# Kernel tuning notes

Hardware: AMD Instinct MI355X
Metric: run time of the kernel (lower is better)

## Reference

```python
import jax, jax.numpy as jnp
import numpy as np

D_MODEL = 1024
N_LAYER = 2
VOCAB = 50257
D_STATE = 64
D_CONV = 4
EXPAND = 2
HEADDIM = 64
D_INNER = EXPAND * D_MODEL            # 2048
NHEADS = D_INNER // HEADDIM           # 32
CONV_DIM = D_INNER + 2 * D_STATE      # x, B, C share the conv (ngroups=1)
D_PROJ = 2 * D_INNER + 2 * D_STATE + NHEADS  # z, xBC, dt
D_FF = 4 * D_MODEL
B, T = 1, 1024
EPS = 1e-5


def _layernorm(x, w):
    mu = jnp.mean(x, -1, keepdims=True)
    v = jnp.mean((x - mu) ** 2, -1, keepdims=True)
    return (x - mu) * jax.lax.rsqrt(v + EPS) * w


def _rmsnorm(x, w):
    return x * jax.lax.rsqrt(jnp.mean(x ** 2, -1, keepdims=True) + EPS) * w


def setup_inputs() -> dict:
    key = jax.random.key(0)
    ks = jax.random.split(key, 16)
    std = 0.02
    idx = jax.random.randint(ks[0], (B, T), 0, VOCAB)
    targets = jax.random.randint(ks[1], (B, T), 0, VOCAB)
    E = jax.random.normal(ks[2], (VOCAB, D_MODEL)) * std  # tied embedding / lm_head
    norm_w = jnp.ones((N_LAYER, D_MODEL))
    norm2_w = jnp.ones((N_LAYER, D_MODEL))
    norm_f_w = jnp.ones((D_MODEL,))
    in_proj_w = jax.random.normal(ks[3], (N_LAYER, D_PROJ, D_MODEL)) * std
    conv_w = jax.random.normal(ks[4], (N_LAYER, CONV_DIM, D_CONV)) / np.sqrt(D_CONV)
    conv_b = jnp.zeros((N_LAYER, CONV_DIM))
    dt = jnp.exp(jax.random.uniform(ks[5], (N_LAYER, NHEADS)) * (np.log(0.1) - np.log(1e-3)) + np.log(1e-3))
    dt_bias = dt + jnp.log(-jnp.expm1(-dt))  # inverse softplus
    A_log = jnp.log(jax.random.uniform(ks[6], (N_LAYER, NHEADS), minval=1.0, maxval=16.0))
    Dp = jnp.ones((N_LAYER, NHEADS))
    gnorm_w = jnp.ones((N_LAYER, D_INNER))
    out_proj_w = jax.random.normal(ks[7], (N_LAYER, D_MODEL, D_INNER)) * std / np.sqrt(2 * N_LAYER)
    fc1_w = jax.random.normal(ks[8], (N_LAYER, 2 * D_FF, D_MODEL)) * std
    fc2_w = jax.random.normal(ks[9], (N_LAYER, D_MODEL, D_FF)) * std / np.sqrt(2 * N_LAYER)
    return {"idx": idx, "targets": targets, "E": E, "norm_w": norm_w, "norm2_w": norm2_w,
            "in_proj_w": in_proj_w, "conv_w": conv_w, "conv_b": conv_b, "dt_bias": dt_bias,
            "A_log": A_log, "Dp": Dp, "gnorm_w": gnorm_w, "out_proj_w": out_proj_w,
            "fc1_w": fc1_w, "fc2_w": fc2_w, "norm_f_w": norm_f_w}


def _mamba2(x, Wi, cw, cb, dtb, Al, Dh, gw, Wo):
    b, l, _ = x.shape
    zxbcdt = x @ Wi.T  # [b,l,D_PROJ]
    z = zxbcdt[..., :D_INNER]
    xBC = zxbcdt[..., D_INNER:D_INNER + CONV_DIM]
    dt = zxbcdt[..., D_INNER + CONV_DIM:]  # [b,l,H]
    # depthwise causal conv1d over time
    xp = jnp.pad(xBC, ((0, 0), (D_CONV - 1, 0), (0, 0)))
    xBC = sum(xp[:, k:k + l, :] * cw[:, k] for k in range(D_CONV)) + cb
    xBC = jax.nn.silu(xBC)
    xs = xBC[..., :D_INNER].reshape(b, l, NHEADS, HEADDIM)
    Bm = xBC[..., D_INNER:D_INNER + D_STATE]  # [b,l,N] (ngroups=1)
    Cm = xBC[..., D_INNER + D_STATE:]
    dt = jax.nn.softplus(dt + dtb)            # [b,l,H]
    dA = jnp.exp(dt * (-jnp.exp(Al)))         # [b,l,H]
    tm = lambda a: jnp.moveaxis(a, 1, 0)      # time-major for scan

    def step(h, inp):
        dA_t, dt_t, x_t, B_t, C_t = inp
        h = dA_t[..., None, None] * h + jnp.einsum('bh,bhp,bn->bhpn', dt_t, x_t, B_t)
        return h, jnp.einsum('bhpn,bn->bhp', h, C_t)

    h0 = jnp.zeros((b, NHEADS, HEADDIM, D_STATE), x.dtype)
    _, ys = jax.lax.scan(step, h0, (tm(dA), tm(dt), tm(xs), tm(Bm), tm(Cm)))
    y = jnp.moveaxis(ys, 0, 1) + Dh[None, None, :, None] * xs  # skip term D*x
    y = y.reshape(b, l, D_INNER)
    y = _rmsnorm(y * jax.nn.silu(z), gw)  # gated RMSNorm
    return y @ Wo.T


def _gated_mlp(x, W1, W2):
    y = x @ W1.T
    y, g = jnp.split(y, 2, axis=-1)
    return (y * jax.nn.silu(g)) @ W2.T


def reference(idx, targets, E, norm_w, norm2_w, in_proj_w, conv_w, conv_b, dt_bias,
              A_log, Dp, gnorm_w, out_proj_w, fc1_w, fc2_w, norm_f_w):
    h = E[idx]  # [B,T,D]
    for i in range(N_LAYER):
        x = _layernorm(h, norm_w[i])
        x = _mamba2(x, in_proj_w[i], conv_w[i], conv_b[i], dt_bias[i], A_log[i],
                    Dp[i], gnorm_w[i], out_proj_w[i])
        res = x + h
        x = _layernorm(res, norm2_w[i])
        h = _gated_mlp(x, fc1_w[i], fc2_w[i]) + res
    h = _layernorm(h, norm_f_w)
    logits = h @ E.T  # tied lm_head
    logp = jax.nn.log_softmax(logits, axis=-1)
    nll = -jnp.take_along_axis(logp, targets[..., None], axis=-1)[..., 0]
    loss = jnp.mean(nll)  # no ignore_index=-1 entries present
    return logits, loss
```

## Files before the change

kernel.cpp:

```cpp
#include <hip/hip_runtime.h>
#include <cmath>

#define DMODEL  1024
#define DINNER  2048
#define NHEADS  32
#define CONVDIM 2176
#define DPROJ   4256
#define VOCAB   50257
#define NBLK_V  400
#define VOCABP  (NBLK_V * 128)
#define CLEN    16
#define NCHUNK  64

typedef float f32x4 __attribute__((ext_vector_type(4)));
typedef float f32x2 __attribute__((ext_vector_type(2)));
typedef unsigned short u16;
typedef u16 u16x4 __attribute__((ext_vector_type(4)));
typedef u16 u16x8 __attribute__((ext_vector_type(8)));
typedef __bf16 bf16x8 __attribute__((ext_vector_type(8)));

__device__ __forceinline__ u16 f2bf(float f) {
  unsigned u = __builtin_bit_cast(unsigned, f);
  u += 0x7FFFu + ((u >> 16) & 1u);
  return (u16)(u >> 16);
}
__device__ __forceinline__ float silu_f(float x) { return x / (1.f + expf(-x)); }

__device__ __forceinline__ void gload16(const u16* g, u16* l) {
  __builtin_amdgcn_global_load_lds(
      (const __attribute__((address_space(1))) void*)g,
      (__attribute__((address_space(3))) void*)l,
      16, 0, 0);
}

__global__ __launch_bounds__(256) void gemm_bf16(
    const u16* __restrict__ A, const u16* __restrict__ B,
    float* __restrict__ C, int N, int K, int kslice,
    float* __restrict__ lsepart, int swz, int nblk,
    u16* __restrict__ glu_out)
{
  __shared__ alignas(128) u16 As[2][128 * 64];
  __shared__ alignas(128) u16 Bs[2][128 * 64];
  const int tid = threadIdx.x;
  int m0, n0;
  if (swz) {
    int bid = blockIdx.x;
    m0 = ((bid >> 3) & 7) << 7;
    n0 = ((bid & 7) + ((bid >> 6) << 3)) << 7;
  } else {
    m0 = blockIdx.x << 7;
    n0 = blockIdx.y << 7;
  }
  const int lane = tid & 63, wid = tid >> 6;
  const int wm = (wid >> 1) << 6, wn = (wid & 1) << 6;
  const int lr = lane & 15, kg = lane >> 4;

  const int srow = wid * 8 + (lane >> 3);
  const int scol = ((lane & 7) ^ (lane >> 3)) << 3;
  const u16* gA = A + (size_t)(m0 + srow) * K + scol;
  const u16* gB = B + (size_t)(n0 + srow) * K + scol;

  f32x4 acc[4][4];
#pragma unroll
  for (int i = 0; i < 4; ++i)
#pragma unroll
    for (int j = 0; j < 4; ++j) acc[i][j] = (f32x4){0.f, 0.f, 0.f, 0.f};

  const int kb = blockIdx.z * kslice;
  const int nt = kslice >> 6;

  auto stage = [&](int buf, int kk) {
#pragma unroll
    for (int i = 0; i < 4; ++i) {
      gload16(gA + kk + (size_t)i * 32 * K, &As[buf][i * 2048 + wid * 512]);
      gload16(gB + kk + (size_t)i * 32 * K, &Bs[buf][i * 2048 + wid * 512]);
    }
  };

  stage(0, kb);
  asm volatile("s_waitcnt vmcnt(0)" ::: "memory");
  __builtin_amdgcn_s_barrier();

  int cur = 0;
  for (int t = 0; t < nt; ++t) {
    if (t + 1 < nt) stage(cur ^ 1, kb + (t + 1) * 64);
#pragma unroll
    for (int kk = 0; kk < 2; ++kk) {
      bf16x8 af[4], bfr[4];
      const int cx = ((kk * 4 + kg) ^ (lr & 7)) << 3;
#pragma unroll
      for (int f = 0; f < 4; ++f) {
        af[f]  = *(const bf16x8*)&As[cur][(wm + f * 16 + lr) * 64 + cx];
        bfr[f] = *(const bf16x8*)&Bs[cur][(wn + f * 16 + lr) * 64 + cx];
      }
#pragma unroll
      for (int i = 0; i < 4; ++i)
#pragma unroll
        for (int j = 0; j < 4; ++j)
          acc[i][j] = __builtin_amdgcn_mfma_f32_16x16x32_bf16(af[i], bfr[j], acc[i][j], 0, 0, 0);
    }
    asm volatile("s_waitcnt vmcnt(0)" ::: "memory");
    __builtin_amdgcn_s_barrier();
    cur ^= 1;
  }

  const int mr = (lane >> 4) << 2;
  const int nc = lane & 15;

  if (glu_out) {
#pragma unroll
    for (int i = 0; i < 4; ++i)
#pragma unroll
      for (int j = 0; j < 4; ++j)
#pragma unroll
        for (int e = 0; e < 4; ++e) {
          float v = acc[i][j][e];
          float p = __shfl_xor(v, 1);
          if (!(nc & 1)) {
            int q = (n0 + wn + j * 16 + nc) >> 1;
            int row = m0 + wm + i * 16 + mr + e;
            glu_out[(size_t)row * 4096 + q] = f2bf(v * silu_f(p));
          }
        }
    return;
  }

  float* Cw = C + (gridDim.z > 1 ? (size_t)blockIdx.z * 1024 * N : 0);
#pragma unroll
  for (int i = 0; i < 4; ++i)
#pragma unroll
    for (int j = 0; j < 4; ++j) {
      int n = n0 + wn + j * 16 + nc;
      if (n < N) {
#pragma unroll
        for (int e = 0; e < 4; ++e)
          Cw[(size_t)(m0 + wm + i * 16 + mr + e) * N + n] = acc[i][j][e];
      }
    }

  if (lsepart) {
    float* Ls = (float*)As;
#pragma unroll
    for (int i = 0; i < 4; ++i)
#pragma unroll
      for (int e = 0; e < 4; ++e) {
        float pm = -1e30f;
#pragma unroll
        for (int j = 0; j < 4; ++j) {
          int n = n0 + wn + j * 16 + nc;
          if (n < N) pm = fmaxf(pm, acc[i][j][e]);
        }
#pragma unroll
        for (int o = 1; o < 16; o <<= 1) pm = fmaxf(pm, __shfl_xor(pm, o));
        float ps = 0.f;
#pragma unroll
        for (int j = 0; j < 4; ++j) {
          int n = n0 + wn + j * 16 + nc;
          if (n < N) ps += expf(acc[i][j][e] - pm);
        }
#pragma unroll
        for (int o = 1; o < 16; o <<= 1) ps += __shfl_xor(ps, o);
        if (nc == 0) {
          int row = wm + i * 16 + mr + e;
          Ls[row * 4 + (wid & 1) * 2] = pm;
          Ls[row * 4 + (wid & 1) * 2 + 1] = ps;
        }
      }
    __syncthreads();
    if (tid < 128) {
      float pa = Ls[tid * 4], sa = Ls[tid * 4 + 1];
      float pb = Ls[tid * 4 + 2], sb = Ls[tid * 4 + 3];
      float M = fmaxf(pa, pb);
      float S = sa * expf(pa - M) + sb * expf(pb - M);
      ((f32x2*)lsepart)[(size_t)(m0 + tid) * nblk + (n0 >> 7)] = (f32x2){M, S};
    }
  }
}

__global__ void k_cvt8(const float* __restrict__ src, u16* __restrict__ dst, int n8) {
  int i = blockIdx.x * 256 + threadIdx.x;
  if (i >= n8) return;
  f32x4 a = ((const f32x4*)src)[i * 2];
  f32x4 b = ((const f32x4*)src)[i * 2 + 1];
  u16x8 o = { f2bf(a[0]), f2bf(a[1]), f2bf(a[2]), f2bf(a[3]),
              f2bf(b[0]), f2bf(b[1]), f2bf(b[2]), f2bf(b[3]) };
  ((u16x8*)dst)[i] = o;
}

__global__ void k_cvt8_pad(const float* __restrict__ src, u16* __restrict__ dst,
                           int n8, int srcN8) {
  int i = blockIdx.x * 256 + threadIdx.x;
  if (i >= n8) return;
  u16x8 o;
  if (i < srcN8) {
    f32x4 a = ((const f32x4*)src)[i * 2];
    f32x4 b = ((const f32x4*)src)[i * 2 + 1];
    o = (u16x8){ f2bf(a[0]), f2bf(a[1]), f2bf(a[2]), f2bf(a[3]),
                 f2bf(b[0]), f2bf(b[1]), f2bf(b[2]), f2bf(b[3]) };
  } else {
    o = (u16x8){0, 0, 0, 0, 0, 0, 0, 0};
  }
  ((u16x8*)dst)[i] = o;
}

__global__ void k_cvt_fc1(const float* __restrict__ src, u16* __restrict__ dst, int n8) {
  int i = blockIdx.x * 256 + threadIdx.x;
  if (i >= n8) return;
  f32x4 a = ((const f32x4*)src)[i * 2];
  f32x4 b = ((const f32x4*)src)[i * 2 + 1];
  u16x8 o = { f2bf(a[0]), f2bf(a[1]), f2bf(a[2]), f2bf(a[3]),
              f2bf(b[0]), f2bf(b[1]), f2bf(b[2]), f2bf(b[3]) };
  int R = i >> 7, col8 = i & 127;
  int layer = R >> 13, r = R & 8191;
  int dstr = (r < 4096) ? (r << 1) : (((r - 4096) << 1) | 1);
  ((u16x8*)dst)[((size_t)(layer << 13) + dstr) * 128 + col8] = o;
}

__device__ __forceinline__ void ln_write(f32x4 v, const float* __restrict__ w,
                                         u16* __restrict__ out, int t, int tid) {
  float s = v[0] + v[1] + v[2] + v[3];
  float sq = v[0]*v[0] + v[1]*v[1] + v[2]*v[2] + v[3]*v[3];
#pragma unroll
  for (int o = 32; o; o >>= 1) { s += __shfl_down(s, o); sq += __shfl_down(sq, o); }
  __shared__ float sb[4], qb[4];
  if ((tid & 63) == 0) { sb[tid >> 6] = s; qb[tid >> 6] = sq; }
  __syncthreads();
  s = sb[0] + sb[1] + sb[2] + sb[3];
  sq = qb[0] + qb[1] + qb[2] + qb[3];
  float mu = s * (1.f / 1024.f);
  float rstd = rsqrtf(sq * (1.f / 1024.f) - mu * mu + 1e-5f);
  u16x4 o;
#pragma unroll
  for (int e = 0; e < 4; ++e) o[e] = f2bf((v[e] - mu) * rstd * w[tid * 4 + e]);
  ((u16x4*)out)[t * 256 + tid] = o;
}

__global__ void k_ln_embed(const int* __restrict__ idx, const float* __restrict__ E,
                           const float* __restrict__ w, float* __restrict__ hbuf,
                           u16* __restrict__ out) {
  int t = blockIdx.x, tid = threadIdx.x;
  f32x4 v = ((const f32x4*)(E + (size_t)idx[t] * DMODEL))[tid];
  ((f32x4*)hbuf)[t * 256 + tid] = v;
  ln_write(v, w, out, t, tid);
}

__global__ void k_red_ln(const float* __restrict__ part, int S,
                         float* __restrict__ hbuf, const float* __restrict__ w,
                         u16* __restrict__ out) {
  int t = blockIdx.x, tid = threadIdx.x;
  f32x4 v = ((const f32x4*)hbuf)[t * 256 + tid];
  for (int k = 0; k < S; ++k)
    v += ((const f32x4*)part)[(size_t)k * 262144 + t * 256 + tid];
  ((f32x4*)hbuf)[t * 256 + tid] = v;
  ln_write(v, w, out, t, tid);
}

__global__ void k_convdt(const float* __restrict__ zx, const float* __restrict__ cw,
                         const float* __restrict__ cb, const float* __restrict__ dtb,
                         const float* __restrict__ alog, float* __restrict__ xbc,
                         float* __restrict__ dtsp, float* __restrict__ dag) {
  int t = blockIdx.y, x = blockIdx.x, tid = threadIdx.x;
  if (x < 8 || tid < 128) {
    int c = x * 256 + tid;
    float acc = cb[c];
#pragma unroll
    for (int k = 0; k < 4; ++k) {
      int tt = t + k - 3;
      if (tt >= 0) acc += zx[(size_t)tt * DPROJ + 2048 + c] * cw[c * 4 + k];
    }
    xbc[(size_t)t * CONVDIM + c] = silu_f(acc);
  } else if (tid < 160) {
    int hh = tid - 128;
    float raw = zx[(size_t)t * DPROJ + 4224 + hh] + dtb[hh];
    float sp = raw > 20.f ? raw : log1pf(expf(raw));
    dtsp[t * 32 + hh] = sp;
    dag[t * 32 + hh] = expf(-expf(alog[hh]) * sp);
  }
}

__global__ __launch_bounds__(256) void k_scan_local(
    const float* __restrict__ xbc, const float* __restrict__ dtsp,
    const float* __restrict__ dag, float* __restrict__ yb, float* __restrict__ Sloc,
    float* __restrict__ pref, float* __restrict__ dacum)
{
  int c = blockIdx.x, hh = blockIdx.y;
  int tid = threadIdx.x;
  int p = tid >> 2, ng = tid & 3, n0 = ng << 4;
  float st[16];
#pragma unroll
  for (int j = 0; j < 16; ++j) st[j] = 0.f;
  float P = 1.f;
  for (int s_ = 0; s_ < CLEN; ++s_) {
    int t = c * CLEN + s_;
    float dA = dag[t * 32 + hh];
    P *= dA;
    if (tid == 0) pref[t * 32 + hh] = P;
    float coef = dtsp[t * 32 + hh] * xbc[(size_t)t * CONVDIM + hh * 64 + p];
    const f32x4* B4 = (const f32x4*)&xbc[(size_t)t * CONVDIM + 2048 + n0];
    const f32x4* C4 = (const f32x4*)&xbc[(size_t)t * CONVDIM + 2112 + n0];
    float y = 0.f;
#pragma unroll
    for (int q = 0; q < 4; ++q) {
      f32x4 b = B4[q], cc = C4[q];
#pragma unroll
      for (int e = 0; e < 4; ++e) {
        int j = q * 4 + e;
        st[j] = dA * st[j] + coef * b[e];
        y += st[j] * cc[e];
      }
    }
    y += __shfl_xor(y, 1);
    y += __shfl_xor(y, 2);
    if (ng == 0) yb[(size_t)t * DINNER + hh * 64 + p] = y;
  }
  if (tid == 0) dacum[c * 32 + hh] = P;
  float* Sp = Sloc + ((size_t)(c * 32 + hh) * 64 + p) * 64 + n0;
#pragma unroll
  for (int q = 0; q < 4; ++q)
    *(f32x4*)(Sp + q * 4) = (f32x4){ st[q*4], st[q*4+1], st[q*4+2], st[q*4+3] };
}

__global__ void k_chain(const float* __restrict__ Sloc, const float* __restrict__ dacum,
                        float* __restrict__ Sin) {
  int e = blockIdx.x * 256 + threadIdx.x;
  int hh = e >> 12;
  float S = 0.f;
  for (int c = 0; c < NCHUNK; ++c) {
    Sin[(size_t)c * 131072 + e] = S;
    S = dacum[c * 32 + hh] * S + Sloc[(size_t)c * 131072 + e];
  }
}

__global__ __launch_bounds__(256) void k_scan_fix(
    const float* __restrict__ xbc, const float* __restrict__ pref,
    const float* __restrict__ Sin, const float* __restrict__ Dp,
    float* __restrict__ yb)
{
  __shared__ float Sl[64 * 68];
  int c = blockIdx.x, hh = blockIdx.y;
  int tid = threadIdx.x;
  for (int i = 0; i < 16; ++i) {
    int e = i * 256 + tid;
    Sl[(e >> 6) * 68 + (e & 63)] = Sin[(size_t)(c * 32 + hh) * 4096 + e];
  }
  __syncthreads();
  int p = tid >> 2, ng = tid & 3, n0 = ng << 4;
  float Dh = Dp[hh];
  for (int s_ = 0; s_ < CLEN; ++s_) {
    int t = c * CLEN + s_;
    const f32x4* C4 = (const f32x4*)&xbc[(size_t)t * CONVDIM + 2112 + n0];
    float yc = 0.f;
#pragma unroll
    for (int q = 0; q < 4; ++q) {
      f32x4 cc = C4[q];
#pragma unroll
      for (int e = 0; e < 4; ++e) yc += Sl[p * 68 + n0 + q * 4 + e] * cc[e];
    }
    yc += __shfl_xor(yc, 1);
    yc += __shfl_xor(yc, 2);
    if (ng == 0) {
      size_t oy = (size_t)t * DINNER + hh * 64 + p;
      yb[oy] = yb[oy] + pref[t * 32 + hh] * yc + Dh * xbc[(size_t)t * CONVDIM + hh * 64 + p];
    }
  }
}

__global__ void k_gated_rms(const float* __restrict__ yb, const float* __restrict__ zx,
                            const float* __restrict__ gw, u16* __restrict__ out) {
  int t = blockIdx.x, tid = threadIdx.x;
  float v[8], ss = 0.f;
#pragma unroll
  for (int i = 0; i < 8; ++i) {
    int j = tid + i * 256;
    float z = zx[(size_t)t * DPROJ + j];
    float vv = yb[(size_t)t * DINNER + j] * silu_f(z);
    v[i] = vv; ss += vv * vv;
  }
#pragma unroll
  for (int o = 32; o; o >>= 1) ss += __shfl_down(ss, o);
  __shared__ float sb[4];
  if ((tid & 63) == 0) sb[tid >> 6] = ss;
  __syncthreads();
  ss = sb[0] + sb[1] + sb[2] + sb[3];
  float rstd = rsqrtf(ss * (1.f / 2048.f) + 1e-5f);
#pragma unroll
  for (int i = 0; i < 8; ++i) {
    int j = tid + i * 256;
    out[(size_t)t * DINNER + j] = f2bf(v[i] * rstd * gw[j]);
  }
}

__global__ void k_loss_final(const float* __restrict__ lsepart,
                             const float* __restrict__ logits,
                             const int* __restrict__ tgt, float* __restrict__ part) {
  int t = blockIdx.x, tid = threadIdx.x;
  float m = -1e30f, s = 0.f;
  for (int nb = tid; nb < NBLK_V; nb += 256) {
    f32x2 v = ((const f32x2*)lsepart)[(size_t)t * NBLK_V + nb];
    float M = fmaxf(m, v[0]);
    s = s * expf(m - M) + v[1] * expf(v[0] - M);
    m = M;
  }
#pragma unroll
  for (int o = 32; o; o >>= 1) {
    float m2 = __shfl_down(m, o), s2 = __shfl_down(s, o);
    float M = fmaxf(m, m2);
    s = s * expf(m - M) + s2 * expf(m2 - M);
    m = M;
  }
  __shared__ float ms[4], ssh[4];
  if ((tid & 63) == 0) { ms[tid >> 6] = m; ssh[tid >> 6] = s; }
  __syncthreads();
  if (tid == 0) {
    float M = ms[0], S = ssh[0];
    for (int w = 1; w < 4; ++w) {
      float M2 = fmaxf(M, ms[w]);
      S = S * expf(M - M2) + ssh[w] * expf(ms[w] - M2);
      M = M2;
    }
    part[t] = (M + logf(S)) - logits[(size_t)t * VOCAB + tgt[t]];
  }
}

__global__ void k_loss_mean(const float* __restrict__ part, float* __restrict__ out) {
  int tid = threadIdx.x;
  float s = 0.f;
  for (int j = tid; j < 1024; j += 256) s += part[j];
#pragma unroll
  for (int o = 32; o; o >>= 1) s += __shfl_down(s, o);
  __shared__ float sb[4];
  if ((tid & 63) == 0) sb[tid >> 6] = s;
  __syncthreads();
  if (tid == 0) out[0] = (sb[0] + sb[1] + sb[2] + sb[3]) * (1.f / 1024.f);
}

extern "C" void kernel_launch(void* const* d_in, const int* in_sizes, int n_in,
                              void* d_out, int out_size, void* d_ws, size_t ws_size,
                              hipStream_t stream)
{
  const int*   idx       = (const int*)d_in[0];
  const int*   tgt       = (const int*)d_in[1];
  const float* E         = (const float*)d_in[2];
  const float* norm_w    = (const float*)d_in[3];
  const float* norm2_w   = (const float*)d_in[4];
  const float* in_proj_w = (const float*)d_in[5];
  const float* conv_w    = (const float*)d_in[6];
  const float* conv_b    = (const float*)d_in[7];
  const float* dt_bias   = (const float*)d_in[8];
  const float* A_log     = (const float*)d_in[9];
  const float* Dp        = (const float*)d_in[10];
  const float* gnorm_w   = (const float*)d_in[11];
  const float* out_proj_w= (const float*)d_in[12];
  const float* fc1_w     = (const float*)d_in[13];
  const float* fc2_w     = (const float*)d_in[14];
  const float* norm_f_w  = (const float*)d_in[15];
  float* logits = (float*)d_out;
  (void)in_sizes; (void)n_in; (void)out_size; (void)ws_size;

  char* W = (char*)d_ws;
  size_t off = 0;
  auto A8 = [&](size_t bytes) { void* p = W + off; off = (off + bytes + 255) & ~(size_t)255; return p; };
  float* hbuf   = (float*)A8((size_t)1024 * 1024 * 4);
  u16*   xnormb = (u16*)  A8((size_t)1024 * 1024 * 2);
  u16*   gatedb = (u16*)  A8((size_t)1024 * 2048 * 2);
  u16*   glub   = (u16*)  A8((size_t)1024 * 4096 * 2);
  float* dtsp   = (float*)A8((size_t)1024 * 32 * 4);
  float* dag    = (float*)A8((size_t)1024 * 32 * 4);
  float* pref   = (float*)A8((size_t)1024 * 32 * 4);
  float* dacum  = (float*)A8((size_t)2048 * 4);
  float* lpart  = (float*)A8((size_t)1024 * 4);
  float* lsebuf = (float*)A8((size_t)1024 * NBLK_V * 2 * 4);
  u16*   wip    = (u16*)  A8((size_t)2 * 4352 * 1024 * 2);
  u16*   wop    = (u16*)  A8((size_t)2 * 1024 * 2048 * 2);
  u16*   wfc1   = (u16*)  A8((size_t)2 * 8192 * 1024 * 2);
  u16*   wfc2   = (u16*)  A8((size_t)2 * 1024 * 4096 * 2);
  char*  span   = (char*)A8((size_t)117964800);
  float* big0   = (float*)(span);
  float* xbc    = (float*)(span + 33554432);
  float* yb     = (float*)(span + 33554432 + 8912896);
  float* Sloc   = (float*)(span + 33554432 + 8912896 + 8388608);
  float* Sin    = (float*)((char*)Sloc + 33554432);
  float* part   = Sloc;
  u16*   Ebf    = (u16*)span;

  dim3 b256(256);

  k_cvt8_pad<<<dim3((4352*1024/8 + 255)/256), b256, 0, stream>>>(
      in_proj_w, wip, 4352*1024/8, 4256*1024/8);
  k_cvt8_pad<<<dim3((4352*1024/8 + 255)/256), b256, 0, stream>>>(
      in_proj_w + (size_t)4256*1024, wip + (size_t)4352*1024, 4352*1024/8, 4256*1024/8);
  k_cvt8<<<dim3(2*1024*2048/8/256), b256, 0, stream>>>(out_proj_w, wop, 2*1024*2048/8);
  k_cvt_fc1<<<dim3(2*8192*1024/8/256), b256, 0, stream>>>(fc1_w, wfc1, 2*8192*1024/8);
  k_cvt8<<<dim3(2*1024*4096/8/256), b256, 0, stream>>>(fc2_w, wfc2, 2*1024*4096/8);

  k_ln_embed<<<1024, b256, 0, stream>>>(idx, E, norm_w, hbuf, xnormb);

  const float* nw_next[2] = { norm_w + 1024, norm_f_w };
  for (int L = 0; L < 2; ++L) {
    gemm_bf16<<<dim3(8, 34, 1), b256, 0, stream>>>(
        xnormb, wip + (size_t)L * 4352 * 1024, big0, DPROJ, 1024, 1024,
        nullptr, 0, 34, nullptr);
    k_convdt<<<dim3(9, 1024), b256, 0, stream>>>(
        big0, conv_w + L * CONVDIM * 4, conv_b + L * CONVDIM,
        dt_bias + L * 32, A_log + L * 32, xbc, dtsp, dag);
    k_scan_local<<<dim3(64, 32), b256, 0, stream>>>(xbc, dtsp, dag, yb, Sloc, pref, dacum);
    k_chain<<<512, b256, 0, stream>>>(Sloc, dacum, Sin);
    k_scan_fix<<<dim3(64, 32), b256, 0, stream>>>(xbc, pref, Sin, Dp + L * 32, yb);
    k_gated_rms<<<1024, b256, 0, stream>>>(yb, big0, gnorm_w + L * 2048, gatedb);
    gemm_bf16<<<dim3(8, 8, 2), b256, 0, stream>>>(
        gatedb, wop + (size_t)L * 1024 * 2048, part, 1024, 2048, 1024,
        nullptr, 0, 8, nullptr);
    k_red_ln<<<1024, b256, 0, stream>>>(part, 2, hbuf, norm2_w + L * 1024, xnormb);
    gemm_bf16<<<dim3(8, 64, 1), b256, 0, stream>>>(
        xnormb, wfc1 + (size_t)L * 8192 * 1024, nullptr, 8192, 1024, 1024,
        nullptr, 0, 64, glub);
    gemm_bf16<<<dim3(8, 8, 4), b256, 0, stream>>>(
        glub, wfc2 + (size_t)L * 1024 * 4096, part, 1024, 4096, 1024,
        nullptr, 0, 8, nullptr);
    k_red_ln<<<1024, b256, 0, stream>>>(part, 4, hbuf, nw_next[L], xnormb);
  }

  k_cvt8_pad<<<dim3((VOCABP*1024/8 + 255)/256), b256, 0, stream>>>(
      E, Ebf, VOCABP*1024/8, VOCAB*1024/8);
  gemm_bf16<<<dim3(8 * NBLK_V, 1, 1), b256, 0, stream>>>(
      xnormb, Ebf, logits, VOCAB, 1024, 1024, lsebuf, 1, NBLK_V, nullptr);
  k_loss_final<<<1024, b256, 0, stream>>>(lsebuf, logits, tgt, lpart);
  k_loss_mean<<<1, b256, 0, stream>>>(lpart, logits + (size_t)1024 * VOCAB);
}
```

Baseline: 837.2 us.

## Triple-buffer GEMM with BK=32 stages, deepen split-K, batch chain loads

```diff
diff --git a/kernel.cpp b/kernel.cpp
--- a/kernel.cpp
+++ b/kernel.cpp
@@ -39,8 +39,8 @@
     float* __restrict__ lsepart, int swz, int nblk,
     u16* __restrict__ glu_out)
 {
-  __shared__ alignas(128) u16 As[2][128 * 64];
-  __shared__ alignas(128) u16 Bs[2][128 * 64];
+  __shared__ alignas(128) u16 As[3 * 4096];
+  __shared__ alignas(128) u16 Bs[3 * 4096];
   const int tid = threadIdx.x;
   int m0, n0;
   if (swz) {
@@ -55,8 +55,8 @@
   const int wm = (wid >> 1) << 6, wn = (wid & 1) << 6;
   const int lr = lane & 15, kg = lane >> 4;
 
-  const int srow = wid * 8 + (lane >> 3);
-  const int scol = ((lane & 7) ^ (lane >> 3)) << 3;
+  const int srow = wid * 16 + (lane >> 2);
+  const int scol = ((lane & 3) ^ ((lane >> 3) & 3)) << 3;
   const u16* gA = A + (size_t)(m0 + srow) * K + scol;
   const u16* gB = B + (size_t)(n0 + srow) * K + scol;
 
@@ -67,41 +67,39 @@
     for (int j = 0; j < 4; ++j) acc[i][j] = (f32x4){0.f, 0.f, 0.f, 0.f};
 
   const int kb = blockIdx.z * kslice;
-  const int nt = kslice >> 6;
-
-  auto stage = [&](int buf, int kk) {
-#pragma unroll
-    for (int i = 0; i < 4; ++i) {
-      gload16(gA + kk + (size_t)i * 32 * K, &As[buf][i * 2048 + wid * 512]);
-      gload16(gB + kk + (size_t)i * 32 * K, &Bs[buf][i * 2048 + wid * 512]);
+  const int nt = kslice >> 5;
+
+  auto stage = [&](int buf, int t) {
+    const int ko = kb + (t << 5);
+#pragma unroll
+    for (int i = 0; i < 2; ++i) {
+      gload16(gA + ko + (size_t)i * 64 * K, &As[buf * 4096 + i * 2048 + wid * 512]);
+      gload16(gB + ko + (size_t)i * 64 * K, &Bs[buf * 4096 + i * 2048 + wid * 512]);
     }
   };
 
-  stage(0, kb);
-  asm volatile("s_waitcnt vmcnt(0)" ::: "memory");
-  __builtin_amdgcn_s_barrier();
-
-  int cur = 0;
+  stage(0, 0);
+  stage(1, 1);
+  int b0 = 0, b1 = 1, b2 = 2;
+  const int cxr = ((lr >> 1) & 3);
   for (int t = 0; t < nt; ++t) {
-    if (t + 1 < nt) stage(cur ^ 1, kb + (t + 1) * 64);
-#pragma unroll
-    for (int kk = 0; kk < 2; ++kk) {
-      bf16x8 af[4], bfr[4];
-      const int cx = ((kk * 4 + kg) ^ (lr & 7)) << 3;
-#pragma unroll
-      for (int f = 0; f < 4; ++f) {
-        af[f]  = *(const bf16x8*)&As[cur][(wm + f * 16 + lr) * 64 + cx];
-        bfr[f] = *(const bf16x8*)&Bs[cur][(wn + f * 16 + lr) * 64 + cx];
-      }
-#pragma unroll
-      for (int i = 0; i < 4; ++i)
-#pragma unroll
-        for (int j = 0; j < 4; ++j)
-          acc[i][j] = __builtin_amdgcn_mfma_f32_16x16x32_bf16(af[i], bfr[j], acc[i][j], 0, 0, 0);
-    }
-    asm volatile("s_waitcnt vmcnt(0)" ::: "memory");
+    if (t == nt - 1) asm volatile("s_waitcnt vmcnt(0)" ::: "memory");
+    else             asm volatile("s_waitcnt vmcnt(4)" ::: "memory");
     __builtin_amdgcn_s_barrier();
-    cur ^= 1;
+    if (t + 2 < nt) stage(b2, t + 2);
+    bf16x8 af[4], bfr[4];
+#pragma unroll
+    for (int f = 0; f < 4; ++f) {
+      const int po = ((kg ^ cxr) << 3);
+      af[f]  = *(const bf16x8*)&As[b0 * 4096 + (wm + f * 16 + lr) * 32 + po];
+      bfr[f] = *(const bf16x8*)&Bs[b0 * 4096 + (wn + f * 16 + lr) * 32 + po];
+    }
+#pragma unroll
+    for (int i = 0; i < 4; ++i)
+#pragma unroll
+      for (int j = 0; j < 4; ++j)
+        acc[i][j] = __builtin_amdgcn_mfma_f32_16x16x32_bf16(af[i], bfr[j], acc[i][j], 0, 0, 0);
+    int tmp = b0; b0 = b1; b1 = b2; b2 = tmp;
   }
 
   const int mr = (lane >> 4) << 2;
@@ -139,6 +137,7 @@
     }
 
   if (lsepart) {
+    __syncthreads();
     float* Ls = (float*)As;
 #pragma unroll
     for (int i = 0; i < 4; ++i)
@@ -325,9 +324,17 @@
   int e = blockIdx.x * 256 + threadIdx.x;
   int hh = e >> 12;
   float S = 0.f;
-  for (int c = 0; c < NCHUNK; ++c) {
-    Sin[(size_t)c * 131072 + e] = S;
-    S = dacum[c * 32 + hh] * S + Sloc[(size_t)c * 131072 + e];
+  for (int c = 0; c < NCHUNK; c += 8) {
+    float sl[8], dd[8];
+#pragma unroll
+    for (int j = 0; j < 8; ++j) sl[j] = Sloc[(size_t)(c + j) * 131072 + e];
+#pragma unroll
+    for (int j = 0; j < 8; ++j) dd[j] = dacum[(c + j) * 32 + hh];
+#pragma unroll
+    for (int j = 0; j < 8; ++j) {
+      Sin[(size_t)(c + j) * 131072 + e] = S;
+      S = dd[j] * S + sl[j];
+    }
   }
 }
 
@@ -507,17 +514,17 @@
     k_chain<<<512, b256, 0, stream>>>(Sloc, dacum, Sin);
     k_scan_fix<<<dim3(64, 32), b256, 0, stream>>>(xbc, pref, Sin, Dp + L * 32, yb);
     k_gated_rms<<<1024, b256, 0, stream>>>(yb, big0, gnorm_w + L * 2048, gatedb);
-    gemm_bf16<<<dim3(8, 8, 2), b256, 0, stream>>>(
-        gatedb, wop + (size_t)L * 1024 * 2048, part, 1024, 2048, 1024,
+    gemm_bf16<<<dim3(8, 8, 4), b256, 0, stream>>>(
+        gatedb, wop + (size_t)L * 1024 * 2048, part, 1024, 2048, 512,
         nullptr, 0, 8, nullptr);
-    k_red_ln<<<1024, b256, 0, stream>>>(part, 2, hbuf, norm2_w + L * 1024, xnormb);
+    k_red_ln<<<1024, b256, 0, stream>>>(part, 4, hbuf, norm2_w + L * 1024, xnormb);
     gemm_bf16<<<dim3(8, 64, 1), b256, 0, stream>>>(
         xnormb, wfc1 + (size_t)L * 8192 * 1024, nullptr, 8192, 1024, 1024,
         nullptr, 0, 64, glub);
-    gemm_bf16<<<dim3(8, 8, 4), b256, 0, stream>>>(
-        glub, wfc2 + (size_t)L * 1024 * 4096, part, 1024, 4096, 1024,
+    gemm_bf16<<<dim3(8, 8, 8), b256, 0, stream>>>(
+        glub, wfc2 + (size_t)L * 1024 * 4096, part, 1024, 4096, 512,
         nullptr, 0, 8, nullptr);
-    k_red_ln<<<1024, b256, 0, stream>>>(part, 4, hbuf, nw_next[L], xnormb);
+    k_red_ln<<<1024, b256, 0, stream>>>(part, 8, hbuf, nw_next[L], xnormb);
   }
 
   k_cvt8_pad<<<dim3((VOCABP*1024/8 + 255)/256), b256, 0, stream>>>(
```

Result: no change. 823.9 us (-1.6%).
